# Performance work log

Hardware: AMD Instinct MI355X
Metric: run time of the kernel (lower is better)

## Reference

```python
import jax, jax.numpy as jnp
import numpy as np

B, T, C = 16, 8192, 256
E, K = 8, 2
CAPACITY = int(T / E * 1.25)  # 1280, per (row, expert) token capacity
DFF = 4 * C


def setup_inputs() -> dict:
    key = jax.random.key(0)
    ks = jax.random.split(key, 8)
    s = 0.02
    return {
        "x": jax.random.normal(ks[0], (B, T, C), jnp.float32),
        "rW1": jax.random.normal(ks[1], (C, DFF), jnp.float32) * s,
        "rb1": jnp.zeros((DFF,), jnp.float32),
        "rW2": jax.random.normal(ks[2], (DFF, DFF), jnp.float32) * s,
        "rb2": jnp.zeros((DFF,), jnp.float32),
        "rW3": jax.random.normal(ks[3], (DFF, E), jnp.float32) * s,
        "rb3": jnp.zeros((E,), jnp.float32),
        "eWi": jax.random.normal(ks[4], (E, C, DFF), jnp.float32) * s,
        "ebi": jnp.zeros((E, DFF), jnp.float32),
        "eWo": jax.random.normal(ks[5], (E, DFF, C), jnp.float32) * s,
        "ebo": jnp.zeros((E, C), jnp.float32),
    }


def _row_kept_mask(cnt):
    # Mask over per-row token *ranks*: which of the cnt routed tokens survive capacity.
    # Over capacity: torch.linspace(0, cnt-1, CAPACITY).int() subsampling.
    cnt_f = cnt.astype(jnp.float32)
    lin = jnp.floor(jnp.arange(CAPACITY, dtype=jnp.float32) * (cnt_f - 1.0) / (CAPACITY - 1)).astype(jnp.int32)
    m_lin = jnp.zeros((T,), bool).at[jnp.clip(lin, 0, T - 1)].set(True)
    m_all = jnp.arange(T) < cnt
    return jnp.where(cnt > CAPACITY, m_lin, m_all)


def reference(x, rW1, rb1, rW2, rb2, rW3, rb3, eWi, ebi, eWo, ebo):
    # Router MLP (dropout = identity in eval) + softmax
    h = jax.nn.relu(x @ rW1 + rb1)
    h = jax.nn.relu(h @ rW2 + rb2)
    probs = jax.nn.softmax(h @ rW3 + rb3, axis=-1)          # [B,T,E]
    topk_probs, topk_experts = jax.lax.top_k(probs, K)      # [B,T,K]

    out = jnp.zeros_like(x)
    rows = jnp.arange(B)[:, None]
    for e in range(E):
        sel_k = topk_experts == e                            # [B,T,K]
        sel = sel_k.any(-1)                                  # [B,T] token routed to e
        w = (topk_probs * sel_k).sum(-1)                     # [B,T] gate weight
        count = sel.sum(-1)                                  # [B]
        rank = jnp.cumsum(sel, axis=1) - 1                   # [B,T] rank within row (t-sorted)
        kept_by_rank = jax.vmap(_row_kept_mask)(count)       # [B,T]
        kept = sel & jnp.take_along_axis(kept_by_rank, jnp.clip(rank, 0, T - 1), axis=1)
        # gather up to CAPACITY kept tokens per row (stable keeps t order)
        idx = jnp.argsort(~kept, axis=1, stable=True)[:, :CAPACITY]       # [B,cap]
        valid = jnp.take_along_axis(kept, idx, axis=1)                    # [B,cap]
        toks = jnp.take_along_axis(x, idx[..., None], axis=1)             # [B,cap,C]
        y = jax.nn.relu(toks @ eWi[e] + ebi[e]) @ eWo[e] + ebo[e]         # expert FFN
        gate = valid * jnp.take_along_axis(w, idx, axis=1)                # [B,cap]
        out = out.at[rows, idx].add(y * gate[..., None])
    return out


if __name__ == "__main__":
    print(reference(**setup_inputs()).shape)
```

## Files before the change

kernel.cpp:

```cpp
#include <hip/hip_runtime.h>
#include <hip/hip_bf16.h>
#include <stdint.h>

namespace {

constexpr int TT    = 8192;
constexpr int BB    = 16;
constexpr int CD    = 256;
constexpr int FD    = 1024;
constexpr int CAPY  = 1280;
constexpr int NTOK  = BB * TT;
constexpr int NPAIR = BB * 8;
constexpr int FLAGCAP1 = 16384;
constexpr int FLAGCAP2 = 4096;
constexpr int TPC   = 32768;
constexpr int NCHUNK = NTOK / TPC;

using f4 = float4;
typedef __attribute__((ext_vector_type(8))) short short8;
typedef __attribute__((ext_vector_type(8))) _Float16 half8;
typedef __attribute__((ext_vector_type(4))) float f32x4;

#define MFMA_BF __builtin_amdgcn_mfma_f32_16x16x32_bf16
#define MFMA_HF __builtin_amdgcn_mfma_f32_16x16x32_f16

__device__ __forceinline__ f4 ld4(const float* p){ return *(const f4*)p; }

__device__ __forceinline__ unsigned short bfh(float x){
  uint32_t u = __float_as_uint(x);
  return (unsigned short)((u + 0x7fffu + ((u >> 16) & 1u)) >> 16);
}
__device__ __forceinline__ float b2f(unsigned short h){
  return __uint_as_float(((uint32_t)h) << 16);
}
__device__ __forceinline__ uint32_t packbf(float x){
  uint32_t u = __float_as_uint(x);
  uint32_t hi = (u + 0x7fffu + ((u >> 16) & 1u)) & 0xffff0000u;
  float r = x - __uint_as_float(hi);
  uint32_t v = __float_as_uint(r);
  uint32_t lo = ((v + 0x7fffu + ((v >> 16) & 1u)) >> 16) & 0xffffu;
  return hi | lo;
}
__device__ __forceinline__ unsigned short f16b(float v){
  union { _Float16 h; unsigned short u; } U; U.h = (_Float16)v; return U.u;
}
__device__ __forceinline__ void unpack8(const uint32_t* p, short8& h, short8& l){
  uint4 a = *(const uint4*)p;
  uint4 b = *(const uint4*)(p + 4);
  union { uint32_t u[4]; short8 s; } H, L;
  H.u[0] = (a.y & 0xffff0000u) | (a.x >> 16);  L.u[0] = (a.y << 16) | (a.x & 0xffffu);
  H.u[1] = (a.w & 0xffff0000u) | (a.z >> 16);  L.u[1] = (a.w << 16) | (a.z & 0xffffu);
  H.u[2] = (b.y & 0xffff0000u) | (b.x >> 16);  L.u[2] = (b.y << 16) | (b.x & 0xffffu);
  H.u[3] = (b.w & 0xffff0000u) | (b.z >> 16);  L.u[3] = (b.w << 16) | (b.z & 0xffffu);
  h = H.s; l = L.s;
}

__device__ __forceinline__ void gload16(const unsigned short* g, unsigned short* l){
  __builtin_amdgcn_global_load_lds(
      (const __attribute__((address_space(1))) void*)reinterpret_cast<uintptr_t>(g),
      (__attribute__((address_space(3))) void*)(uint32_t)reinterpret_cast<uintptr_t>(l),
      16, 0, 0);
}

__global__ __launch_bounds__(256)
void prep_transpose(const float* __restrict__ in, unsigned short* __restrict__ oh,
                    unsigned short* __restrict__ ol, int R, int C)
{
  __shared__ float T[32][33];
  const int tx = threadIdx.x & 31, ty = threadIdx.x >> 5;
  const size_t bs = (size_t)R * C;
  const float* ib = in + bs * blockIdx.z;
  unsigned short* ohb = oh + bs * blockIdx.z;
  unsigned short* olb = ol + bs * blockIdx.z;
  const int r0 = blockIdx.y * 32, c0 = blockIdx.x * 32;
  #pragma unroll
  for (int j = 0; j < 4; ++j)
    T[ty + 8*j][tx] = ib[(size_t)(r0 + ty + 8*j)*C + c0 + tx];
  __syncthreads();
  #pragma unroll
  for (int j = 0; j < 4; ++j){
    float v = T[tx][ty + 8*j];
    unsigned short h = bfh(v);
    unsigned short lo = bfh(v - b2f(h));
    size_t o = (size_t)(c0 + ty + 8*j)*R + r0 + tx;
    ohb[o] = h; olb[o] = lo;
  }
}

__global__ __launch_bounds__(256)
void prep_transpose_f16(const float* __restrict__ in, unsigned short* __restrict__ o, int R, int C)
{
  __shared__ float T[32][33];
  const int tx = threadIdx.x & 31, ty = threadIdx.x >> 5;
  const size_t bs = (size_t)R * C;
  const float* ib = in + bs * blockIdx.z;
  unsigned short* ob = o + bs * blockIdx.z;
  const int r0 = blockIdx.y * 32, c0 = blockIdx.x * 32;
  #pragma unroll
  for (int j = 0; j < 4; ++j)
    T[ty + 8*j][tx] = ib[(size_t)(r0 + ty + 8*j)*C + c0 + tx];
  __syncthreads();
  #pragma unroll
  for (int j = 0; j < 4; ++j)
    ob[(size_t)(c0 + ty + 8*j)*R + r0 + tx] = f16b(T[tx][ty + 8*j]);
}

__global__ __launch_bounds__(256)
void gemm_a(const float* __restrict__ x, int tok0,
            const unsigned short* __restrict__ W1F,
            const float* __restrict__ b1,
            unsigned short* __restrict__ H1)
{
  __shared__ unsigned short smem[16384];
  unsigned short* As = smem;
  unsigned short* Bs = smem + 8192;
  const int tid = threadIdx.x;
  const int w = tid >> 6, lane = tid & 63, l15 = lane & 15, l4 = lane >> 4;
  const int wm = w >> 1, wn = w & 1;
  const int mt0 = (blockIdx.x >> 3) * 128;
  const int nt0 = (blockIdx.x & 7) * 128;
  const int row_s = tid >> 1, half = tid & 1;
  const int lrow = lane >> 3;
  const int srcB = lrow*CD + (((lane & 7) ^ lrow) << 3);

  f32x4 acc[4][4];
  #pragma unroll
  for (int mt = 0; mt < 4; ++mt)
    #pragma unroll
    for (int nt = 0; nt < 4; ++nt)
      acc[mt][nt] = (f32x4){0.f,0.f,0.f,0.f};

  #pragma unroll 1
  for (int ks = 0; ks < 4; ++ks){
    {
      const unsigned short* bbase = W1F + (size_t)nt0*CD + ks*64;
      #pragma unroll
      for (int i = 0; i < 4; ++i){
        const int r0 = w*32 + i*8;
        gload16(bbase + (size_t)r0*CD + srcB, Bs + r0*64);
      }
    }
    const float* asrc = x + (size_t)(tok0 + mt0 + row_s)*CD + ks*64 + half*32;
    f4 av[8];
    #pragma unroll
    for (int j = 0; j < 8; ++j) av[j] = ld4(asrc + j*4);
    #pragma unroll
    for (int j = 0; j < 4; ++j){
      union { unsigned short u[8]; short8 s; } U;
      f4 p = av[2*j], q = av[2*j+1];
      U.u[0]=f16b(p.x); U.u[1]=f16b(p.y); U.u[2]=f16b(p.z); U.u[3]=f16b(p.w);
      U.u[4]=f16b(q.x); U.u[5]=f16b(q.y); U.u[6]=f16b(q.z); U.u[7]=f16b(q.w);
      const int g = half*4 + j;
      *(short8*)&As[row_s*64 + ((g ^ (row_s & 7)) << 3)] = U.s;
    }
    __syncthreads();
    #pragma unroll
    for (int kt = 0; kt < 2; ++kt){
      half8 af[4], bf[4];
      #pragma unroll
      for (int mt = 0; mt < 4; ++mt){
        const int r = 64*wm + 16*mt + l15;
        af[mt] = *(const half8*)&As[r*64 + (((kt*4 + l4) ^ (r & 7)) << 3)];
      }
      #pragma unroll
      for (int nt = 0; nt < 4; ++nt){
        const int r = 64*wn + 16*nt + l15;
        bf[nt] = *(const half8*)&Bs[r*64 + (((kt*4 + l4) ^ (r & 7)) << 3)];
      }
      #pragma unroll
      for (int mt = 0; mt < 4; ++mt)
        #pragma unroll
        for (int nt = 0; nt < 4; ++nt)
          acc[mt][nt] = MFMA_HF(af[mt], bf[nt], acc[mt][nt], 0,0,0);
    }
    __syncthreads();
  }

  unsigned short* Cs = smem;
  #pragma unroll
  for (int nt = 0; nt < 4; ++nt){
    const int ncol = 64*wn + 16*nt + l15;
    const float b1v = b1[nt0 + ncol];
    #pragma unroll
    for (int mt = 0; mt < 4; ++mt)
      #pragma unroll
      for (int r = 0; r < 4; ++r){
        const int tr = 64*wm + 16*mt + 4*l4 + r;
        Cs[tr*128 + ncol] = f16b(fmaxf(acc[mt][nt][r] + b1v, 0.f));
      }
  }
  __syncthreads();
  {
    unsigned short* dst = H1 + (size_t)(mt0 + row_s)*FD + nt0 + half*64;
    const unsigned short* src = Cs + row_s*128 + half*64;
    #pragma unroll
    for (int j = 0; j < 8; ++j) ((uint4*)dst)[j] = ((const uint4*)src)[j];
  }
}

__global__ __launch_bounds__(256, 2)
void gemm_b(const unsigned short* __restrict__ H1, int tok0,
            const unsigned short* __restrict__ W2F,
            const float* __restrict__ b2,
            const float* __restrict__ W3,
            float* __restrict__ plg)
{
  __shared__ unsigned short smem[16384];
  unsigned short* As = smem;
  unsigned short* Bs = smem + 8192;
  const int tid = threadIdx.x;
  const int w = tid >> 6, lane = tid & 63, l15 = lane & 15, l4 = lane >> 4;
  const int wm = w >> 1, wn = w & 1;
  const int ntile = blockIdx.x & 7;
  const int mt0 = (blockIdx.x >> 3) * 128;
  const int nt0 = ntile * 128;
  const int row_s = tid >> 1, half = tid & 1;
  const int lrow = lane >> 3;
  const int srcAB = lrow*FD + (((lane & 7) ^ lrow) << 3);

  f32x4 acc[4][4];
  #pragma unroll
  for (int mt = 0; mt < 4; ++mt)
    #pragma unroll
    for (int nt = 0; nt < 4; ++nt)
      acc[mt][nt] = (f32x4){0.f,0.f,0.f,0.f};

  #pragma unroll 1
  for (int ks = 0; ks < 16; ++ks){
    const unsigned short* abase = H1  + (size_t)mt0*FD + ks*64;
    const unsigned short* bbase = W2F + (size_t)nt0*FD + ks*64;
    #pragma unroll
    for (int i = 0; i < 4; ++i){
      const int r0 = w*32 + i*8;
      gload16(abase + (size_t)r0*FD + srcAB, As + r0*64);
      gload16(bbase + (size_t)r0*FD + srcAB, Bs + r0*64);
    }
    __syncthreads();
    #pragma unroll
    for (int kt = 0; kt < 2; ++kt){
      half8 af[4], bf[4];
      #pragma unroll
      for (int mt = 0; mt < 4; ++mt){
        const int r = 64*wm + 16*mt + l15;
        af[mt] = *(const half8*)&As[r*64 + (((kt*4 + l4) ^ (r & 7)) << 3)];
      }
      #pragma unroll
      for (int nt = 0; nt < 4; ++nt){
        const int r = 64*wn + 16*nt + l15;
        bf[nt] = *(const half8*)&Bs[r*64 + (((kt*4 + l4) ^ (r & 7)) << 3)];
      }
      #pragma unroll
      for (int mt = 0; mt < 4; ++mt)
        #pragma unroll
        for (int nt = 0; nt < 4; ++nt)
          acc[mt][nt] = MFMA_HF(af[mt], bf[nt], acc[mt][nt], 0,0,0);
    }
    __syncthreads();
  }

  float* lgs = (float*)smem;
  *(f4*)&lgs[tid*4] = (f4){0.f,0.f,0.f,0.f};
  __syncthreads();

  #pragma unroll
  for (int mt = 0; mt < 4; ++mt){
    float lp[4][8];
    #pragma unroll
    for (int r = 0; r < 4; ++r)
      #pragma unroll
      for (int e = 0; e < 8; ++e) lp[r][e] = 0.f;
    #pragma unroll
    for (int nt = 0; nt < 4; ++nt){
      const int n2 = nt0 + 64*wn + 16*nt + l15;
      const float b2v = b2[n2];
      f4 wa = ld4(W3 + n2*8), wb3 = ld4(W3 + n2*8 + 4);
      const float w3s[8] = {wa.x,wa.y,wa.z,wa.w,wb3.x,wb3.y,wb3.z,wb3.w};
      #pragma unroll
      for (int r = 0; r < 4; ++r){
        float h2 = fmaxf(acc[mt][nt][r] + b2v, 0.f);
        #pragma unroll
        for (int e = 0; e < 8; ++e)
          lp[r][e] = fmaf(h2, w3s[e], lp[r][e]);
      }
    }
    #pragma unroll
    for (int off = 1; off < 16; off <<= 1)
      #pragma unroll
      for (int r = 0; r < 4; ++r)
        #pragma unroll
        for (int e = 0; e < 8; ++e)
          lp[r][e] += __shfl_xor(lp[r][e], off);
    if (l15 == 0){
      #pragma unroll
      for (int r = 0; r < 4; ++r){
        const int row = 64*wm + 16*mt + 4*l4 + r;
        #pragma unroll
        for (int e = 0; e < 8; ++e)
          atomicAdd(&lgs[row*8 + e], lp[r][e]);
      }
    }
  }
  __syncthreads();
  {
    f4 v = *(const f4*)&lgs[row_s*8 + half*4];
    *(f4*)(plg + ((size_t)ntile*NTOK + tok0 + mt0 + row_s)*8 + half*4) = v;
  }
}

__global__ __launch_bounds__(256)
void top2_kernel(const float* __restrict__ plg, const float* __restrict__ b3,
                 int2* __restrict__ topE, float2* __restrict__ topW,
                 int* __restrict__ flagList, int* __restrict__ flagCnt)
{
  const int tok = blockIdx.x*256 + threadIdx.x;
  float l[8];
  #pragma unroll
  for (int e = 0; e < 8; ++e) l[e] = b3[e];
  #pragma unroll
  for (int s = 0; s < 8; ++s){
    const float* p = plg + ((size_t)s*NTOK + tok)*8;
    f4 p0 = ld4(p), p1 = ld4(p + 4);
    l[0]+=p0.x; l[1]+=p0.y; l[2]+=p0.z; l[3]+=p0.w;
    l[4]+=p1.x; l[5]+=p1.y; l[6]+=p1.z; l[7]+=p1.w;
  }
  int e1 = 0; float v1 = l[0];
  #pragma unroll
  for (int e = 1; e < 8; ++e){ if (l[e] > v1){ v1 = l[e]; e1 = e; } }
  int e2 = 0; float v2 = -3.0e38f;
  #pragma unroll
  for (int e = 0; e < 8; ++e){ if (e != e1 && l[e] > v2){ v2 = l[e]; e2 = e; } }
  float v3 = -3.0e38f;
  #pragma unroll
  for (int e = 0; e < 8; ++e){ if (e != e1 && e != e2 && l[e] > v3) v3 = l[e]; }
  float s = 0.f;
  #pragma unroll
  for (int e = 0; e < 8; ++e) s += expf(l[e]-v1);
  topE[tok] = make_int2(e1, e2);
  topW[tok] = make_float2(1.0f/s, expf(v2 - v1)/s);
  if (v2 - v3 < 5e-4f){
    int i = atomicAdd(flagCnt, 1);
    if (i < FLAGCAP1) flagList[i] = tok;
  }
}

__global__ __launch_bounds__(512, 2)
void router_fix1(const float* __restrict__ x,
                 const unsigned short* __restrict__ W1Th, const unsigned short* __restrict__ W1Tl,
                 const float* __restrict__ b1,
                 const unsigned short* __restrict__ W2Th, const unsigned short* __restrict__ W2Tl,
                 const float* __restrict__ b2,
                 const float* __restrict__ W3, const float* __restrict__ b3,
                 const int* __restrict__ flagList, const int* __restrict__ flagCnt,
                 int2* __restrict__ topE, float2* __restrict__ topW,
                 int* __restrict__ flagList2, int* __restrict__ flagCnt2)
{
  int cnt = *flagCnt; if (cnt > FLAGCAP1) cnt = FLAGCAP1;
  const int s0 = blockIdx.x * 32;
  if (s0 >= cnt) return;

  __shared__ uint32_t Xp[32*256];
  __shared__ uint32_t Hp[32*128];
  __shared__ float lgs[32*8];
  __shared__ int sTok[32];
  const int tid = threadIdx.x;
  const int w = tid >> 6, lane = tid & 63;
  const int l15 = lane & 15, l4 = lane >> 4;
  const int swz = l15 & 7;

  if (tid < 32){
    const int s = s0 + tid;
    sTok[tid] = (s < cnt) ? flagList[s] : flagList[s0];
  }
  if (tid < 256) lgs[tid] = 0.f;
  __syncthreads();
  {
    const int row = tid >> 4, cb = (tid & 15) * 2;
    const float* rp = x + (size_t)sTok[row]*CD + cb*8;
    #pragma unroll
    for (int g = 0; g < 2; ++g){
      f4 a = ld4(rp + g*8), bq = ld4(rp + g*8 + 4);
      uint32_t* dst = &Xp[row*256 + (((cb + g) ^ (row & 7)) << 3)];
      *(uint4*)dst     = make_uint4(packbf(a.x),packbf(a.y),packbf(a.z),packbf(a.w));
      *(uint4*)(dst+4) = make_uint4(packbf(bq.x),packbf(bq.y),packbf(bq.z),packbf(bq.w));
    }
  }
  __syncthreads();

  f32x4 acc2[2][8];
  #pragma unroll
  for (int mt = 0; mt < 2; ++mt)
    #pragma unroll
    for (int nt = 0; nt < 8; ++nt)
      acc2[mt][nt] = (f32x4){0.f,0.f,0.f,0.f};

  #pragma unroll 1
  for (int kc = 0; kc < 8; ++kc){
    f32x4 acc1[2] = {(f32x4){0,0,0,0},(f32x4){0,0,0,0}};
    const int n1g = kc*128 + 16*w + l15;
    const size_t wb1 = (size_t)n1g * 256;
    #pragma unroll
    for (int kt = 0; kt < 8; ++kt){
      short8 ah[2], al[2];
      #pragma unroll
      for (int mt = 0; mt < 2; ++mt)
        unpack8(&Xp[(mt*16 + l15)*256 + ((((kt<<2) + l4) ^ swz) << 3)], ah[mt], al[mt]);
      const int kb = kt*32 + 8*l4;
      short8 bh = *(const short8*)&W1Th[wb1 + kb];
      short8 bl = *(const short8*)&W1Tl[wb1 + kb];
      #pragma unroll
      for (int mt = 0; mt < 2; ++mt)
        acc1[mt] = MFMA_BF(ah[mt], bh, MFMA_BF(ah[mt], bl, MFMA_BF(al[mt], bh, acc1[mt],0,0,0),0,0,0),0,0,0);
    }
    __syncthreads();
    {
      const float b1v = b1[n1g];
      const int c = 16*w + l15, ch = c >> 3, co = c & 7;
      #pragma unroll
      for (int mt = 0; mt < 2; ++mt)
        #pragma unroll
        for (int r = 0; r < 4; ++r){
          const int row = mt*16 + 4*l4 + r;
          Hp[row*128 + ((ch ^ (row & 7)) << 3) + co] = packbf(fmaxf(acc1[mt][r] + b1v, 0.f));
        }
    }
    __syncthreads();
    #pragma unroll
    for (int kt = 0; kt < 4; ++kt){
      short8 ah[2], al[2];
      #pragma unroll
      for (int mt = 0; mt < 2; ++mt)
        unpack8(&Hp[(mt*16 + l15)*128 + ((((kt<<2) + l4) ^ swz) << 3)], ah[mt], al[mt]);
      const size_t kg = (size_t)(kc*128 + kt*32 + 8*l4);
      #pragma unroll
      for (int nt = 0; nt < 8; ++nt){
        const size_t wb2 = (size_t)(128*w + 16*nt + l15) * 1024 + kg;
        short8 bh = *(const short8*)&W2Th[wb2];
        short8 bl = *(const short8*)&W2Tl[wb2];
        #pragma unroll
        for (int mt = 0; mt < 2; ++mt)
          acc2[mt][nt] = MFMA_BF(ah[mt], bh, MFMA_BF(ah[mt], bl, MFMA_BF(al[mt], bh, acc2[mt][nt],0,0,0),0,0,0),0,0,0);
      }
    }
  }

  #pragma unroll
  for (int mt = 0; mt < 2; ++mt){
    float lp[4][8];
    #pragma unroll
    for (int r = 0; r < 4; ++r)
      #pragma unroll
      for (int e = 0; e < 8; ++e) lp[r][e] = 0.f;
    #pragma unroll
    for (int nt = 0; nt < 8; ++nt){
      const int n2 = 128*w + 16*nt + l15;
      const float b2v = b2[n2];
      f4 wa = ld4(W3 + n2*8), wb3 = ld4(W3 + n2*8 + 4);
      const float w3s[8] = {wa.x,wa.y,wa.z,wa.w,wb3.x,wb3.y,wb3.z,wb3.w};
      #pragma unroll
      for (int r = 0; r < 4; ++r){
        float h2 = fmaxf(acc2[mt][nt][r] + b2v, 0.f);
        #pragma unroll
        for (int e = 0; e < 8; ++e)
          lp[r][e] = fmaf(h2, w3s[e], lp[r][e]);
      }
    }
    #pragma unroll
    for (int off = 1; off < 16; off <<= 1)
      #pragma unroll
      for (int r = 0; r < 4; ++r)
        #pragma unroll
        for (int e = 0; e < 8; ++e)
          lp[r][e] += __shfl_xor(lp[r][e], off);
    if (l15 == 0){
      #pragma unroll
      for (int r = 0; r < 4; ++r){
        const int row = mt*16 + 4*l4 + r;
        #pragma unroll
        for (int e = 0; e < 8; ++e)
          atomicAdd(&lgs[row*8 + e], lp[r][e]);
      }
    }
  }
  __syncthreads();

  if (tid < 32 && s0 + tid < cnt){
    const int tok = sTok[tid];
    float l[8];
    #pragma unroll
    for (int e = 0; e < 8; ++e) l[e] = lgs[tid*8 + e] + b3[e];
    int e1 = 0; float v1 = l[0];
    #pragma unroll
    for (int e = 1; e < 8; ++e){ if (l[e] > v1){ v1 = l[e]; e1 = e; } }
    int e2 = 0; float v2 = -3.0e38f;
    #pragma unroll
    for (int e = 0; e < 8; ++e){ if (e != e1 && l[e] > v2){ v2 = l[e]; e2 = e; } }
    float v3 = -3.0e38f;
    #pragma unroll
    for (int e = 0; e < 8; ++e){ if (e != e1 && e != e2 && l[e] > v3) v3 = l[e]; }
    float s = 0.f;
    #pragma unroll
    for (int e = 0; e < 8; ++e) s += expf(l[e]-v1);
    topE[tok] = make_int2(e1, e2);
    topW[tok] = make_float2(1.0f/s, expf(v2 - v1)/s);
    if (v2 - v3 < 1e-4f){
      int i = atomicAdd(flagCnt2, 1);
      if (i < FLAGCAP2) flagList2[i] = tok;
    }
  }
}

__global__ __launch_bounds__(256)
void router_fixup(const float* __restrict__ x,
                  const float* __restrict__ W1, const float* __restrict__ b1,
                  const float* __restrict__ W2, const float* __restrict__ b2,
                  const float* __restrict__ W3, const float* __restrict__ b3,
                  const int* __restrict__ flagList, const int* __restrict__ flagCnt,
                  int2* __restrict__ topE, float2* __restrict__ topW)
{
  int n = *flagCnt; if (n > FLAGCAP2) n = FLAGCAP2;
  if ((int)blockIdx.x >= n) return;
  const int t = flagList[blockIdx.x];
  __shared__ float xs[256];
  __shared__ float h1[1024];
  __shared__ float h2[1024];
  __shared__ float lgf[8];
  const int tid = threadIdx.x;
  xs[tid] = x[(size_t)t*256 + tid];
  __syncthreads();
  {
    float a0=b1[tid], a1=b1[tid+256], a2=b1[tid+512], a3=b1[tid+768];
    for (int k = 0; k < 256; ++k){
      const float xv = xs[k];
      const float* wr = W1 + (size_t)k*1024;
      a0 = fmaf(xv, wr[tid],     a0);
      a1 = fmaf(xv, wr[tid+256], a1);
      a2 = fmaf(xv, wr[tid+512], a2);
      a3 = fmaf(xv, wr[tid+768], a3);
    }
    h1[tid]=fmaxf(a0,0.f); h1[tid+256]=fmaxf(a1,0.f); h1[tid+512]=fmaxf(a2,0.f); h1[tid+768]=fmaxf(a3,0.f);
  }
  __syncthreads();
  {
    float a0=b2[tid], a1=b2[tid+256], a2=b2[tid+512], a3=b2[tid+768];
    for (int k = 0; k < 1024; ++k){
      const float hv = h1[k];
      const float* wr = W2 + (size_t)k*1024;
      a0 = fmaf(hv, wr[tid],     a0);
      a1 = fmaf(hv, wr[tid+256], a1);
      a2 = fmaf(hv, wr[tid+512], a2);
      a3 = fmaf(hv, wr[tid+768], a3);
    }
    h2[tid]=fmaxf(a0,0.f); h2[tid+256]=fmaxf(a1,0.f); h2[tid+512]=fmaxf(a2,0.f); h2[tid+768]=fmaxf(a3,0.f);
  }
  __syncthreads();
  {
    const int e = tid >> 5, s = tid & 31;
    float p = 0.f;
    for (int k = s*32; k < s*32+32; ++k) p = fmaf(h2[k], W3[(size_t)k*8 + e], p);
    #pragma unroll
    for (int off = 1; off < 32; off <<= 1) p += __shfl_xor(p, off);
    if (s == 0) lgf[e] = p + b3[e];
  }
  __syncthreads();
  if (tid == 0){
    float l[8];
    #pragma unroll
    for (int e=0;e<8;++e) l[e] = lgf[e];
    int e1 = 0; float v1 = l[0];
    #pragma unroll
    for (int e=1;e<8;++e){ if (l[e] > v1){ v1 = l[e]; e1 = e; } }
    int e2 = 0; float v2 = -3.0e38f;
    #pragma unroll
    for (int e=0;e<8;++e){ if (e != e1 && l[e] > v2){ v2 = l[e]; e2 = e; } }
    float s = 0.f;
    #pragma unroll
    for (int e=0;e<8;++e) s += expf(l[e]-v1);
    topE[t] = make_int2(e1, e2);
    topW[t] = make_float2(1.0f/s, expf(v2 - v1)/s);
  }
}

__global__ __launch_bounds__(256)
void route_compact(const int2* __restrict__ topE, const float2* __restrict__ topW,
                   int* __restrict__ listIdx, float* __restrict__ listW, int* __restrict__ kcnt)
{
  const int blk = blockIdx.x;
  const int b = blk >> 3, e = blk & 7;
  const int2* te = topE + (size_t)b*TT;
  const float2* tw = topW + (size_t)b*TT;
  __shared__ unsigned kmask[256];
  __shared__ int wTot[4], wTot2[4];
  __shared__ int s_cnt, s_baseRank, s_baseSlot;
  const int tid = threadIdx.x;
  const int lane = tid & 63, wid = tid >> 6;

  if (tid == 0){ s_cnt = 0; s_baseRank = 0; s_baseSlot = 0; }
  kmask[tid & 255] = 0;
  __syncthreads();

  int c = 0;
  for (int t = tid; t < TT; t += 256){
    int2 v = te[t];
    c += (v.x == e) || (v.y == e);
  }
  #pragma unroll
  for (int off = 32; off; off >>= 1) c += __shfl_xor(c, off);
  if (lane == 0) atomicAdd(&s_cnt, c);
  __syncthreads();
  const int cnt = s_cnt;

  if (cnt > CAPY){
    for (int i = tid; i < CAPY; i += 256){
      float t1 = (float)i * (float)(cnt - 1);
      float t2 = t1 / 1279.0f;
      int r = (int)floorf(t2);
      atomicOr(&kmask[r >> 5], 1u << (r & 31));
    }
  }
  __syncthreads();

  for (int tile = 0; tile < 32; ++tile){
    const int t = tile*256 + tid;
    const int2 v = te[t];
    const bool sel = (v.x == e) || (v.y == e);
    const float2 wv = tw[t];
    const float w = (v.x == e) ? wv.x : wv.y;

    unsigned long long mSel = __ballot(sel);
    const int lpfx = __popcll(mSel & ((1ull << lane) - 1ull));
    if (lane == 0) wTot[wid] = __popcll(mSel);
    __syncthreads();
    int wpfx = 0;
    for (int wdx = 0; wdx < wid; ++wdx) wpfx += wTot[wdx];
    const int rank = s_baseRank + wpfx + lpfx;

    const bool kept = sel && (cnt <= CAPY || ((kmask[rank >> 5] >> (rank & 31)) & 1u));
    unsigned long long mK = __ballot(kept);
    const int lpfx2 = __popcll(mK & ((1ull << lane) - 1ull));
    if (lane == 0) wTot2[wid] = __popcll(mK);
    __syncthreads();
    int wpfx2 = 0;
    for (int wdx = 0; wdx < wid; ++wdx) wpfx2 += wTot2[wdx];
    const int slot = s_baseSlot + wpfx2 + lpfx2;

    if (kept){
      listIdx[(size_t)blk*CAPY + slot] = t;
      listW [(size_t)blk*CAPY + slot] = w;
    }
    __syncthreads();
    if (tid == 0){
      int a = 0, q = 0;
      for (int wdx = 0; wdx < 4; ++wdx){ a += wTot[wdx]; q += wTot2[wdx]; }
      s_baseRank += a; s_baseSlot += q;
    }
    __syncthreads();
  }
  if (tid == 0) kcnt[blk] = s_baseSlot;
}

__global__ __launch_bounds__(512, 2)
void expert_mfma(const float* __restrict__ x,
                 const unsigned short* __restrict__ WiF, const float* __restrict__ ebi,
                 const unsigned short* __restrict__ WoF, const float* __restrict__ ebo,
                 const int* __restrict__ listIdx, const float* __restrict__ listW,
                 const int* __restrict__ kcnt, float* __restrict__ out)
{
  const int q = blockIdx.y;
  const int e = q >> 4, b = q & 15;
  const int pair = b*8 + e;
  const int kc_n = kcnt[pair];
  const int s0 = blockIdx.x * 64;
  if (s0 >= kc_n) return;

  __shared__ unsigned short Xf[64*256];
  __shared__ unsigned short Hf[64*128];
  __shared__ int sTok[64];
  __shared__ float sG[64];
  const int tid = threadIdx.x;
  const int w = tid >> 6, lane = tid & 63;
  const int l15 = lane & 15, l4 = lane >> 4;
  const int swz = l15 & 7;

  if (tid < 64){
    const int s = s0 + tid;
    const bool v = s < kc_n;
    sTok[tid] = v ? listIdx[(size_t)pair*CAPY + s] : -1;
    sG[tid]   = v ? listW [(size_t)pair*CAPY + s] : 0.f;
  }
  __syncthreads();
  {
    const int row = tid >> 3, cb = (tid & 7) * 4;
    int tk = sTok[row]; if (tk < 0) tk = 0;
    const float* rp = x + ((size_t)b*TT + tk)*CD + cb*8;
    #pragma unroll
    for (int g = 0; g < 4; ++g){
      f4 a = ld4(rp + g*8), bq = ld4(rp + g*8 + 4);
      union { unsigned short u[8]; short8 s; } U;
      U.u[0]=f16b(a.x); U.u[1]=f16b(a.y); U.u[2]=f16b(a.z); U.u[3]=f16b(a.w);
      U.u[4]=f16b(bq.x);U.u[5]=f16b(bq.y);U.u[6]=f16b(bq.z);U.u[7]=f16b(bq.w);
      *(short8*)&Xf[row*256 + (((cb + g) ^ (row & 7)) << 3)] = U.s;
    }
  }
  __syncthreads();

  const unsigned short* Wi = WiF + (size_t)e*FD*CD;
  const unsigned short* Wo = WoF + (size_t)e*CD*FD;

  f32x4 accO[4][2];
  #pragma unroll
  for (int mt = 0; mt < 4; ++mt)
    #pragma unroll
    for (int nt = 0; nt < 2; ++nt)
      accO[mt][nt] = (f32x4){0.f,0.f,0.f,0.f};

  #pragma unroll 1
  for (int kc = 0; kc < 8; ++kc){
    f32x4 acc1[4] = {(f32x4){0,0,0,0},(f32x4){0,0,0,0},(f32x4){0,0,0,0},(f32x4){0,0,0,0}};
    const int n1g = kc*128 + 16*w + l15;
    const size_t wbi = (size_t)n1g * 256;
    #pragma unroll
    for (int kt = 0; kt < 8; ++kt){
      half8 av[4];
      #pragma unroll
      for (int mt = 0; mt < 4; ++mt)
        av[mt] = *(const half8*)&Xf[(mt*16 + l15)*256 + ((((kt<<2) + l4) ^ swz) << 3)];
      half8 bf = *(const half8*)&Wi[wbi + kt*32 + 8*l4];
      #pragma unroll
      for (int mt = 0; mt < 4; ++mt)
        acc1[mt] = MFMA_HF(av[mt], bf, acc1[mt], 0,0,0);
    }
    __syncthreads();
    {
      const float biv = ebi[e*FD + n1g];
      const int c = 16*w + l15, ch = c >> 3, co = c & 7;
      #pragma unroll
      for (int mt = 0; mt < 4; ++mt)
        #pragma unroll
        for (int r = 0; r < 4; ++r){
          const int row = mt*16 + 4*l4 + r;
          Hf[row*128 + ((ch ^ (row & 7)) << 3) + co] = f16b(fmaxf(acc1[mt][r] + biv, 0.f));
        }
    }
    __syncthreads();
    #pragma unroll
    for (int kt = 0; kt < 4; ++kt){
      half8 av[4];
      #pragma unroll
      for (int mt = 0; mt < 4; ++mt)
        av[mt] = *(const half8*)&Hf[(mt*16 + l15)*128 + ((((kt<<2) + l4) ^ swz) << 3)];
      const size_t kg = (size_t)(kc*128 + kt*32 + 8*l4);
      #pragma unroll
      for (int nt = 0; nt < 2; ++nt){
        const int n = 32*w + 16*nt + l15;
        half8 bf = *(const half8*)&Wo[(size_t)n*1024 + kg];
        #pragma unroll
        for (int mt = 0; mt < 4; ++mt)
          accO[mt][nt] = MFMA_HF(av[mt], bf, accO[mt][nt], 0,0,0);
      }
    }
  }

  #pragma unroll
  for (int mt = 0; mt < 4; ++mt)
    #pragma unroll
    for (int r = 0; r < 4; ++r){
      const int row = mt*16 + 4*l4 + r;
      const int tk = sTok[row];
      if (tk >= 0){
        const float g = sG[row];
        #pragma unroll
        for (int nt = 0; nt < 2; ++nt){
          const int n = 32*w + 16*nt + l15;
          atomicAdd(out + ((size_t)b*TT + tk)*CD + n, (accO[mt][nt][r] + ebo[e*CD + n]) * g);
        }
      }
    }
}

}

extern "C" void kernel_launch(void* const* d_in, const int* in_sizes, int n_in,
                              void* d_out, int out_size, void* d_ws, size_t ws_size,
                              hipStream_t stream)
{
  const float* x   = (const float*)d_in[0];
  const float* rW1 = (const float*)d_in[1];
  const float* rb1 = (const float*)d_in[2];
  const float* rW2 = (const float*)d_in[3];
  const float* rb2 = (const float*)d_in[4];
  const float* rW3 = (const float*)d_in[5];
  const float* rb3 = (const float*)d_in[6];
  const float* eWi = (const float*)d_in[7];
  const float* ebi = (const float*)d_in[8];
  const float* eWo = (const float*)d_in[9];
  const float* ebo = (const float*)d_in[10];
  (void)in_sizes; (void)n_in; (void)ws_size;

  char* ws = (char*)d_ws;
  size_t off = 0;
  auto carve = [&](size_t bytes)->char*{ char* p = ws + off; off += (bytes + 255) & ~(size_t)255; return p; };
  unsigned short* W1F  = (unsigned short*)carve((size_t)FD*CD*2);
  unsigned short* W2F  = (unsigned short*)carve((size_t)FD*FD*2);
  unsigned short* W1Th = (unsigned short*)carve((size_t)FD*CD*2);
  unsigned short* W1Tl = (unsigned short*)carve((size_t)FD*CD*2);
  unsigned short* W2Th = (unsigned short*)carve((size_t)FD*FD*2);
  unsigned short* W2Tl = (unsigned short*)carve((size_t)FD*FD*2);
  unsigned short* WiF  = (unsigned short*)carve((size_t)8*FD*CD*2);
  unsigned short* WoF  = (unsigned short*)carve((size_t)8*CD*FD*2);
  unsigned short* H1   = (unsigned short*)carve((size_t)TPC*FD*2);
  float*  plg     = (float*)carve((size_t)8*NTOK*8*sizeof(float));
  int2*   topE    = (int2*)carve((size_t)NTOK*sizeof(int2));
  float2* topW    = (float2*)carve((size_t)NTOK*sizeof(float2));
  int*    listIdx = (int*)carve((size_t)NPAIR*CAPY*sizeof(int));
  float*  listW   = (float*)carve((size_t)NPAIR*CAPY*sizeof(float));
  int*    kcnt    = (int*)carve((size_t)NPAIR*sizeof(int));
  int*    flagCnt = (int*)carve(256);
  int*    flagCnt2= (int*)carve(256);
  int*    flagList= (int*)carve((size_t)FLAGCAP1*sizeof(int));
  int*    flagList2=(int*)carve((size_t)FLAGCAP2*sizeof(int));

  float* out = (float*)d_out;
  hipMemsetAsync(out, 0, (size_t)out_size*sizeof(float), stream);
  hipMemsetAsync(flagCnt, 0, sizeof(int), stream);
  hipMemsetAsync(flagCnt2, 0, sizeof(int), stream);

  prep_transpose_f16<<<dim3(32, 8, 1), 256, 0, stream>>>(rW1, W1F, 256, 1024);
  prep_transpose_f16<<<dim3(32,32, 1), 256, 0, stream>>>(rW2, W2F, 1024, 1024);
  prep_transpose<<<dim3(32, 8, 1), 256, 0, stream>>>(rW1, W1Th, W1Tl, 256, 1024);
  prep_transpose<<<dim3(32,32, 1), 256, 0, stream>>>(rW2, W2Th, W2Tl, 1024, 1024);
  prep_transpose_f16<<<dim3(32, 8, 8), 256, 0, stream>>>(eWi, WiF, 256, 1024);
  prep_transpose_f16<<<dim3( 8,32, 8), 256, 0, stream>>>(eWo, WoF, 1024, 256);

  for (int c = 0; c < NCHUNK; ++c){
    gemm_a<<<(TPC/128)*8, 256, 0, stream>>>(x, c*TPC, W1F, rb1, H1);
    gemm_b<<<(TPC/128)*8, 256, 0, stream>>>(H1, c*TPC, W2F, rb2, rW3, plg);
  }
  top2_kernel<<<NTOK/256, 256, 0, stream>>>(plg, rb3, topE, topW, flagList, flagCnt);

  router_fix1<<<FLAGCAP1/32, 512, 0, stream>>>(x, W1Th, W1Tl, rb1, W2Th, W2Tl, rb2,
                                               rW3, rb3, flagList, flagCnt,
                                               topE, topW, flagList2, flagCnt2);
  router_fixup<<<FLAGCAP2, 256, 0, stream>>>(x, rW1, rb1, rW2, rb2, rW3, rb3,
                                             flagList2, flagCnt2, topE, topW);
  route_compact<<<NPAIR, 256, 0, stream>>>(topE, topW, listIdx, listW, kcnt);
  expert_mfma<<<dim3(CAPY/64, 128), 512, 0, stream>>>(x, WiF, ebi, WoF, ebo,
                                                      listIdx, listW, kcnt, out);
}
```

Measured before the change: 1.480 ms.

## Pre-convert x to fp16 and use direct-to-LDS loads in router GEMM A

Adds a pass that converts all of x to fp16 once, so gemm_a can stream both A and B tiles with global_load_lds instead of loading fp32 through registers and converting per tile. gemm_a also gets a launch-bounds occupancy hint. Both router GEMMs remap block indices so consecutive blocks share the same N tile, for better L2 reuse of weights. The trade is an extra full read of x plus a 64MB fp16 write and read back, and more workspace.

```diff
diff --git a/kernel.cpp b/kernel.cpp
--- a/kernel.cpp
+++ b/kernel.cpp
@@ -63,6 +63,21 @@
 }
 
 __global__ __launch_bounds__(256)
+void x_to_f16(const float* __restrict__ x, unsigned short* __restrict__ o)
+{
+  const size_t i = (size_t)blockIdx.x*256 + threadIdx.x;
+  const float* p = x + i*16;
+  f4 a = ld4(p), b = ld4(p+4), c = ld4(p+8), d = ld4(p+12);
+  union { unsigned short u[16]; uint4 q[2]; } U;
+  U.u[0]=f16b(a.x); U.u[1]=f16b(a.y); U.u[2]=f16b(a.z); U.u[3]=f16b(a.w);
+  U.u[4]=f16b(b.x); U.u[5]=f16b(b.y); U.u[6]=f16b(b.z); U.u[7]=f16b(b.w);
+  U.u[8]=f16b(c.x); U.u[9]=f16b(c.y); U.u[10]=f16b(c.z); U.u[11]=f16b(c.w);
+  U.u[12]=f16b(d.x);U.u[13]=f16b(d.y);U.u[14]=f16b(d.z); U.u[15]=f16b(d.w);
+  *(uint4*)(o + i*16)     = U.q[0];
+  *(uint4*)(o + i*16 + 8) = U.q[1];
+}
+
+__global__ __launch_bounds__(256)
 void prep_transpose(const float* __restrict__ in, unsigned short* __restrict__ oh,
                     unsigned short* __restrict__ ol, int R, int C)
 {
@@ -105,8 +120,8 @@
     ob[(size_t)(c0 + ty + 8*j)*R + r0 + tx] = f16b(T[tx][ty + 8*j]);
 }
 
-__global__ __launch_bounds__(256)
-void gemm_a(const float* __restrict__ x, int tok0,
+__global__ __launch_bounds__(256, 2)
+void gemm_a(const unsigned short* __restrict__ xF, int tok0,
             const unsigned short* __restrict__ W1F,
             const float* __restrict__ b1,
             unsigned short* __restrict__ H1)
@@ -117,11 +132,12 @@
   const int tid = threadIdx.x;
   const int w = tid >> 6, lane = tid & 63, l15 = lane & 15, l4 = lane >> 4;
   const int wm = w >> 1, wn = w & 1;
-  const int mt0 = (blockIdx.x >> 3) * 128;
-  const int nt0 = (blockIdx.x & 7) * 128;
+  const int bid = ((int)blockIdx.x & 7) * ((int)gridDim.x >> 3) + ((int)blockIdx.x >> 3);
+  const int mt0 = (bid >> 3) * 128;
+  const int nt0 = (bid & 7) * 128;
   const int row_s = tid >> 1, half = tid & 1;
   const int lrow = lane >> 3;
-  const int srcB = lrow*CD + (((lane & 7) ^ lrow) << 3);
+  const int srcAB = lrow*CD + (((lane & 7) ^ lrow) << 3);
 
   f32x4 acc[4][4];
   #pragma unroll
@@ -132,26 +148,13 @@
 
   #pragma unroll 1
   for (int ks = 0; ks < 4; ++ks){
-    {
-      const unsigned short* bbase = W1F + (size_t)nt0*CD + ks*64;
-      #pragma unroll
-      for (int i = 0; i < 4; ++i){
-        const int r0 = w*32 + i*8;
-        gload16(bbase + (size_t)r0*CD + srcB, Bs + r0*64);
-      }
-    }
-    const float* asrc = x + (size_t)(tok0 + mt0 + row_s)*CD + ks*64 + half*32;
-    f4 av[8];
-    #pragma unroll
-    for (int j = 0; j < 8; ++j) av[j] = ld4(asrc + j*4);
-    #pragma unroll
-    for (int j = 0; j < 4; ++j){
-      union { unsigned short u[8]; short8 s; } U;
-      f4 p = av[2*j], q = av[2*j+1];
-      U.u[0]=f16b(p.x); U.u[1]=f16b(p.y); U.u[2]=f16b(p.z); U.u[3]=f16b(p.w);
-      U.u[4]=f16b(q.x); U.u[5]=f16b(q.y); U.u[6]=f16b(q.z); U.u[7]=f16b(q.w);
-      const int g = half*4 + j;
-      *(short8*)&As[row_s*64 + ((g ^ (row_s & 7)) << 3)] = U.s;
+    const unsigned short* abase = xF  + (size_t)(tok0 + mt0)*CD + ks*64;
+    const unsigned short* bbase = W1F + (size_t)nt0*CD + ks*64;
+    #pragma unroll
+    for (int i = 0; i < 4; ++i){
+      const int r0 = w*32 + i*8;
+      gload16(abase + (size_t)r0*CD + srcAB, As + r0*64);
+      gload16(bbase + (size_t)r0*CD + srcAB, Bs + r0*64);
     }
     __syncthreads();
     #pragma unroll
@@ -211,8 +214,9 @@
   const int tid = threadIdx.x;
   const int w = tid >> 6, lane = tid & 63, l15 = lane & 15, l4 = lane >> 4;
   const int wm = w >> 1, wn = w & 1;
-  const int ntile = blockIdx.x & 7;
-  const int mt0 = (blockIdx.x >> 3) * 128;
+  const int bid = ((int)blockIdx.x & 7) * ((int)gridDim.x >> 3) + ((int)blockIdx.x >> 3);
+  const int ntile = bid & 7;
+  const int mt0 = (bid >> 3) * 128;
   const int nt0 = ntile * 128;
   const int row_s = tid >> 1, half = tid & 1;
   const int lrow = lane >> 3;
@@ -807,6 +811,7 @@
   unsigned short* W2Tl = (unsigned short*)carve((size_t)FD*FD*2);
   unsigned short* WiF  = (unsigned short*)carve((size_t)8*FD*CD*2);
   unsigned short* WoF  = (unsigned short*)carve((size_t)8*CD*FD*2);
+  unsigned short* xF16 = (unsigned short*)carve((size_t)NTOK*CD*2);
   unsigned short* H1   = (unsigned short*)carve((size_t)TPC*FD*2);
   float*  plg     = (float*)carve((size_t)8*NTOK*8*sizeof(float));
   int2*   topE    = (int2*)carve((size_t)NTOK*sizeof(int2));
@@ -824,6 +829,7 @@
   hipMemsetAsync(flagCnt, 0, sizeof(int), stream);
   hipMemsetAsync(flagCnt2, 0, sizeof(int), stream);
 
+  x_to_f16<<<NTOK*CD/16/256, 256, 0, stream>>>(x, xF16);
   prep_transpose_f16<<<dim3(32, 8, 1), 256, 0, stream>>>(rW1, W1F, 256, 1024);
   prep_transpose_f16<<<dim3(32,32, 1), 256, 0, stream>>>(rW2, W2F, 1024, 1024);
   prep_transpose<<<dim3(32, 8, 1), 256, 0, stream>>>(rW1, W1Th, W1Tl, 256, 1024);
@@ -832,7 +838,7 @@
   prep_transpose_f16<<<dim3( 8,32, 8), 256, 0, stream>>>(eWo, WoF, 1024, 256);
 
   for (int c = 0; c < NCHUNK; ++c){
-    gemm_a<<<(TPC/128)*8, 256, 0, stream>>>(x, c*TPC, W1F, rb1, H1);
+    gemm_a<<<(TPC/128)*8, 256, 0, stream>>>(xF16, c*TPC, W1F, rb1, H1);
     gemm_b<<<(TPC/128)*8, 256, 0, stream>>>(H1, c*TPC, W2F, rb2, rW3, plg);
   }
   top2_kernel<<<NTOK/256, 256, 0, stream>>>(plg, rb3, topE, topW, flagList, flagCnt);
```

After: 1.322 ms (median of 3 runs). 1.12x faster.
